# Kernel tuning notes

Measured on AMD Instinct MI355X. Metric: run time of the kernel, lower is better.

Reference implementation:

```python
import jax, jax.numpy as jnp
import numpy as np

N = 16384          # total points
B = 2              # scans; points[:,0] is batch id
K = 16             # knn neighbors (includes self, dist 0)
CH = [4, 16, 16, 32, 32]
EPS = 1e-5


def setup_inputs() -> dict:
    key = jax.random.key(0)
    ks = jax.random.split(key, 1 + len(CH) - 1)
    feat = jax.random.normal(ks[0], (N, 4), dtype=jnp.float32)
    bidx = jnp.repeat(jnp.arange(B, dtype=jnp.float32), N // B)
    points = jnp.concatenate([bidx[:, None], feat], axis=1)  # [N,5]
    inp = {"points": points}
    for i in range(len(CH) - 1):
        in_c, out_c = CH[i], CH[i + 1]
        inp[f"W{i}"] = jax.random.normal(ks[1 + i], (out_c, 2 * in_c), dtype=jnp.float32) * 0.1
        inp[f"b{i}"] = jnp.zeros((out_c,), dtype=jnp.float32)
        inp[f"g{i}"] = jnp.ones((out_c,), dtype=jnp.float32)
        inp[f"t{i}"] = jnp.zeros((out_c,), dtype=jnp.float32)
    return inp


def _knn(pos, bidx, k):
    # batched brute-force knn: mask cross-batch pairs with +inf
    d2 = jnp.sum(pos * pos, axis=-1)
    dist = d2[:, None] + d2[None, :] - 2.0 * (pos @ pos.T)  # [N,N]
    dist = jnp.where(bidx[:, None] == bidx[None, :], dist, jnp.inf)
    return jax.lax.top_k(-dist, k)[1]  # [N,k] indices of nearest


def _edge_conv(x, idx, W, b, g, t):
    # x: [N,C]; idx: [N,k]
    xi = x[:, None, :]                                   # [N,1,C]
    e = jnp.concatenate(
        [jnp.broadcast_to(xi, idx.shape + (x.shape[-1],)), x[idx] - xi], axis=-1
    )                                                    # [N,k,2C]
    h = jnp.einsum('nke,oe->nko', e, W) + b              # [N,k,out]
    mu = h.mean(axis=(0, 1))
    var = h.var(axis=(0, 1))
    h = (h - mu) * jax.lax.rsqrt(var + EPS) * g + t      # batch-norm (train mode)
    return jnp.max(jax.nn.relu(h), axis=1)               # max over neighbors -> [N,out]


def reference(points, W0, b0, g0, t0, W1, b1, g1, t1, W2, b2, g2, t2, W3, b3, g3, t3):
    bidx = points[:, 0].astype(jnp.int32)
    pos = points[:, 1:4]
    idx = _knn(pos, bidx, K)
    x = points[:, 1:]  # [N,4]
    for W, b, g, t in ((W0, b0, g0, t0), (W1, b1, g1, t1), (W2, b2, g2, t2), (W3, b3, g3, t3)):
        x = _edge_conv(x, idx, W, b, g, t)
    return x  # [N,32] == batch_dict['gcn_feature']
```

## Files before the change

kernel.cpp:

```cpp
#include <hip/hip_runtime.h>
#include <math.h>

typedef unsigned long long u64;

#define N_PTS 16384
#define HALF_N 8192
#define KK 16
#define NK (N_PTS * KK)
#define EPSV 1e-5f
#define FINF 0x7f800000u

#define TGRP 32
#define TGC 64
#define QW 2
#define QBLK 8
#define CAP 288

#define OFF_IDX   0u
#define OFF_PC    (1u << 20)
#define OFF_MA    (OFF_PC + N_PTS * 16u)
#define OFF_MB    (OFF_MA + N_PTS * 16u * 4u)
#define OFF_MC    (OFF_MB + N_PTS * 16u * 4u)
#define OFF_PART  (OFF_MC + N_PTS * 32u * 4u)
#define OFF_STATS (OFF_PART + 1024u * 64u * 4u)

__global__ __launch_bounds__(256) void prep_kernel(const float* __restrict__ pts,
                                                   float4* __restrict__ pc) {
    int i = blockIdx.x * 256 + threadIdx.x;
    float x = pts[i * 5 + 1], y = pts[i * 5 + 2], z = pts[i * 5 + 3];
    float d2 = __fadd_rn(__fadd_rn(__fmul_rn(x, x), __fmul_rn(y, y)), __fmul_rn(z, z));
    pc[i] = make_float4(x, y, z, d2);
}

__device__ __forceinline__ unsigned fkey(unsigned u) {
    return u ^ ((unsigned)(((int)u) >> 31) | 0x80000000u);
}

__device__ __forceinline__ void cef32(float& a, float& b) {
    float t = fminf(a, b);
    b = fmaxf(a, b);
    a = t;
}

__device__ __forceinline__ void sort8f(float* b) {
    cef32(b[0], b[1]); cef32(b[2], b[3]); cef32(b[4], b[5]); cef32(b[6], b[7]);
    cef32(b[0], b[2]); cef32(b[1], b[3]); cef32(b[4], b[6]); cef32(b[5], b[7]);
    cef32(b[1], b[2]); cef32(b[5], b[6]);
    cef32(b[0], b[4]); cef32(b[1], b[5]); cef32(b[2], b[6]); cef32(b[3], b[7]);
    cef32(b[2], b[4]); cef32(b[3], b[5]);
    cef32(b[1], b[2]); cef32(b[3], b[4]); cef32(b[5], b[6]);
}

__device__ __forceinline__ void sort16f(float b[16]) {
    sort8f(b); sort8f(b + 8);
#pragma unroll
    for (int j = 0; j < 8; ++j) cef32(b[j], b[15 - j]);
#pragma unroll
    for (int h = 0; h < 16; h += 8) {
        cef32(b[h + 0], b[h + 4]); cef32(b[h + 1], b[h + 5]);
        cef32(b[h + 2], b[h + 6]); cef32(b[h + 3], b[h + 7]);
        cef32(b[h + 0], b[h + 2]); cef32(b[h + 1], b[h + 3]);
        cef32(b[h + 4], b[h + 6]); cef32(b[h + 5], b[h + 7]);
        cef32(b[h + 0], b[h + 1]); cef32(b[h + 2], b[h + 3]);
        cef32(b[h + 4], b[h + 5]); cef32(b[h + 6], b[h + 7]);
    }
}

__global__ __launch_bounds__(256, 8) void tau1_kernel(const float4* __restrict__ pc,
                                                      float* __restrict__ gsubT) {
    const int qb = blockIdx.x >> 5;
    const int g  = blockIdx.x & (TGRP - 1);
    const int n  = qb * 256 + threadIdx.x;
    const int base = (n >= HALF_N) ? HALF_N : 0;
    const float4 p = pc[n];

    float m = __uint_as_float(FINF);
    const int c0 = base + g * TGC;
#pragma unroll 8
    for (int t = 0; t < TGC; ++t) {
        const float4 cp = pc[c0 + t];
        float dot = __fadd_rn(__fadd_rn(__fmul_rn(p.x, cp.x), __fmul_rn(p.y, cp.y)),
                              __fmul_rn(p.z, cp.z));
        float dist = __fsub_rn(__fadd_rn(p.w, cp.w), __fmul_rn(2.0f, dot));
        m = fminf(m, dist);
    }
    gsubT[g * N_PTS + n] = m;
}

__global__ __launch_bounds__(256, 4) void tau2_kernel(const float* __restrict__ gsubT,
                                                      float* __restrict__ tauArr) {
    const int n = blockIdx.x * 256 + threadIdx.x;
    float A[16], B[16];
#pragma unroll
    for (int g = 0; g < 16; ++g) A[g] = gsubT[g * N_PTS + n];
#pragma unroll
    for (int g = 0; g < 16; ++g) B[g] = gsubT[(16 + g) * N_PTS + n];
    sort16f(A);
    sort16f(B);
    float tau = __uint_as_float(0xff800000u);
#pragma unroll
    for (int j = 0; j < 16; ++j) tau = fmaxf(tau, fminf(A[j], B[15 - j]));
    tauArr[n] = tau;
}

__global__ __launch_bounds__(256, 8) void collect_kernel(const float4* __restrict__ pc,
                                                         const float* __restrict__ tauArr,
                                                         int* __restrict__ idx) {
    __shared__ u64 lists[QBLK][CAP];

    const int tid  = threadIdx.x;
    const int lane = tid & 63;
    const int w    = tid >> 6;
    const int nb   = blockIdx.x * QBLK + w * QW;
    const int base = (blockIdx.x >= (HALF_N / QBLK)) ? HALF_N : 0;

    const float4 q0 = pc[nb + 0], q1 = pc[nb + 1];
    const float tau0 = tauArr[nb + 0], tau1 = tauArr[nb + 1];

    u64* l0 = lists[w * QW + 0];
    u64* l1 = lists[w * QW + 1];
    int c0 = 0, c1 = 0;

    const u64 lt = (1ull << lane) - 1ull;

    for (int t0 = 0; t0 < HALF_N; t0 += 64) {
        const int ci = base + t0 + lane;
        const float4 cp = pc[ci];

#define DIST(Q) (__fsub_rn(__fadd_rn(Q.w, cp.w), __fmul_rn(2.0f,                      \
            __fadd_rn(__fadd_rn(__fmul_rn(Q.x, cp.x), __fmul_rn(Q.y, cp.y)),          \
                      __fmul_rn(Q.z, cp.z)))))
        const float d0 = DIST(q0);
        const float d1 = DIST(q1);
#undef DIST

#define APPEND(D, TAU, LST, CNT)                                                      \
        {                                                                             \
            const bool acc = !((D) > (TAU));                                          \
            const u64 mask = __ballot(acc);                                           \
            if (mask) {                                                               \
                if (acc) {                                                            \
                    int slot = (CNT) + (int)__popcll(mask & lt);                      \
                    if (slot < CAP)                                                   \
                        (LST)[slot] = ((u64)fkey(__float_as_uint(D)) << 32) | (unsigned)ci; \
                }                                                                     \
                (CNT) += (int)__popcll(mask);                                         \
            }                                                                         \
        }
        APPEND(d0, tau0, l0, c0)
        APPEND(d1, tau1, l1, c1)
#undef APPEND
    }

#define SELECT(LST, CNT, QI)                                                          \
    {                                                                                 \
        const int K = min((CNT), CAP);                                                \
        for (int e = lane; e < K; e += 64) {                                          \
            u64 my = (LST)[e];                                                        \
            int rank = 0;                                                             \
            for (int i = 0; i < K; ++i) rank += ((LST)[i] < my) ? 1 : 0;              \
            if (rank < 16) idx[(nb + (QI)) * KK + rank] = (int)(my & 0xffffffffULL);  \
        }                                                                             \
    }
    SELECT(l0, c0, 0)
    SELECT(l1, c1, 1)
#undef SELECT
}

template <int IN_C, int OUT_C, int MODE>
__global__ __launch_bounds__(256) void convS_kernel(const float* __restrict__ xin,
                                                    const float* __restrict__ statsPrev,
                                                    const int* __restrict__ idxg,
                                                    const float* __restrict__ W,
                                                    const float* __restrict__ bb,
                                                    float* __restrict__ part,
                                                    float* __restrict__ mout) {
    constexpr int RED = 256 / OUT_C;
    __shared__ float hbuf[OUT_C][257];
    __shared__ float pr1[OUT_C][RED + 1];
    __shared__ float pr2[OUT_C][RED + 1];
    __shared__ float2 sAB[IN_C];

    const int tid = threadIdx.x;
    const int gt = blockIdx.x * 256 + tid;
    const int n = gt >> 4;

    if (MODE == 1) {
        if (tid < IN_C) sAB[tid] = make_float2(statsPrev[tid], statsPrev[32 + tid]);
        __syncthreads();
    }

    float xn[IN_C], dx[IN_C];
    const int j = idxg[gt];
    if (MODE == 0) {
        const float* rn = xin + n * 5 + 1;
        const float* rj = xin + j * 5 + 1;
#pragma unroll
        for (int e = 0; e < IN_C; ++e) xn[e] = rn[e];
#pragma unroll
        for (int e = 0; e < IN_C; ++e) dx[e] = rj[e] - xn[e];
    } else {
        const float4* rn = (const float4*)(xin + n * IN_C);
        const float4* rj = (const float4*)(xin + j * IN_C);
#pragma unroll
        for (int e4 = 0; e4 < IN_C / 4; ++e4) {
            float4 a = rn[e4];
            float4 bq = rj[e4];
            float av[4] = {a.x, a.y, a.z, a.w};
            float bv[4] = {bq.x, bq.y, bq.z, bq.w};
#pragma unroll
            for (int u = 0; u < 4; ++u) {
                float2 ab = sAB[4 * e4 + u];
                float xv = fmaxf(fmaf(av[u], ab.x, ab.y), 0.f);
                float jv = fmaxf(fmaf(bv[u], ab.x, ab.y), 0.f);
                xn[4 * e4 + u] = xv;
                dx[4 * e4 + u] = jv - xv;
            }
        }
    }

    float h[OUT_C];
#pragma unroll
    for (int c = 0; c < OUT_C; ++c) {
        float acc = bb[c];
#pragma unroll
        for (int e = 0; e < IN_C; ++e) acc = fmaf(W[c * 2 * IN_C + e], xn[e], acc);
#pragma unroll
        for (int e = 0; e < IN_C; ++e) acc = fmaf(W[c * 2 * IN_C + IN_C + e], dx[e], acc);
        h[c] = acc;
    }

#pragma unroll
    for (int c = 0; c < OUT_C; ++c) hbuf[c][tid] = h[c];
    __syncthreads();
    {
        const int c2 = tid & (OUT_C - 1);
        const int ch = tid / OUT_C;
        float s1 = 0.f, s2 = 0.f;
#pragma unroll
        for (int i = 0; i < OUT_C; ++i) {
            float hh = hbuf[c2][ch * OUT_C + i];
            s1 += hh; s2 += hh * hh;
        }
        pr1[c2][ch] = s1;
        pr2[c2][ch] = s2;
    }
    __syncthreads();
    if (tid < OUT_C) {
        float t1 = 0.f, t2 = 0.f;
#pragma unroll
        for (int k = 0; k < RED; ++k) { t1 += pr1[tid][k]; t2 += pr2[tid][k]; }
        part[blockIdx.x * 64 + tid]      = t1;
        part[blockIdx.x * 64 + 32 + tid] = t2;
    }

    {
        const int n0 = blockIdx.x * 16;
        constexpr int ITER = OUT_C / 16;
#pragma unroll
        for (int r = 0; r < ITER; ++r) {
            const int c = tid & (OUT_C - 1);
            const int nl = (tid / OUT_C) + r * (256 / OUT_C);
            float m = hbuf[c][nl * 16];
#pragma unroll
            for (int k = 1; k < 16; ++k) m = fmaxf(m, hbuf[c][nl * 16 + k]);
            mout[(n0 + nl) * OUT_C + c] = m;
        }
    }
}

__global__ __launch_bounds__(256) void finalize_kernel(const float* __restrict__ part,
                                                       const float* __restrict__ g,
                                                       const float* __restrict__ t,
                                                       float* __restrict__ statsL) {
    __shared__ float s1[128], s2[128];
    const int c = blockIdx.x;
    const int tid = threadIdx.x;

    if (tid < 128) {
        float a = 0.f;
#pragma unroll
        for (int i = 0; i < 8; ++i) a += part[(tid * 8 + i) * 64 + c];
        s1[tid] = a;
    } else {
        const int t2 = tid - 128;
        float a = 0.f;
#pragma unroll
        for (int i = 0; i < 8; ++i) a += part[(t2 * 8 + i) * 64 + 32 + c];
        s2[t2] = a;
    }
    __syncthreads();
    for (int st = 64; st >= 1; st >>= 1) {
        if (tid < st) s1[tid] += s1[tid + st];
        else if (tid >= 128 && tid < 128 + st) s2[tid - 128] += s2[tid - 128 + st];
        __syncthreads();
    }
    if (tid == 0) {
        const float inv = 1.0f / (float)NK;
        float mu  = s1[0] * inv;
        float var = s2[0] * inv - mu * mu;
        float rs  = 1.0f / sqrtf(var + EPSV);
        float A   = rs * g[c];
        statsL[c]      = A;
        statsL[32 + c] = t[c] - mu * A;
    }
}

__global__ __launch_bounds__(256) void apply_kernel(const float* __restrict__ m,
                                                    const float* __restrict__ st,
                                                    float* __restrict__ out) {
    const int i = blockIdx.x * 256 + threadIdx.x;
    float4 mv = ((const float4*)m)[i];
    const int c0 = (i * 4) & 31;
    float4 Av = *(const float4*)(st + c0);
    float4 Bv = *(const float4*)(st + 32 + c0);
    float4 o;
    o.x = fmaxf(fmaf(mv.x, Av.x, Bv.x), 0.f);
    o.y = fmaxf(fmaf(mv.y, Av.y, Bv.y), 0.f);
    o.z = fmaxf(fmaf(mv.z, Av.z, Bv.z), 0.f);
    o.w = fmaxf(fmaf(mv.w, Av.w, Bv.w), 0.f);
    ((float4*)out)[i] = o;
}

extern "C" void kernel_launch(void* const* d_in, const int* in_sizes, int n_in,
                              void* d_out, int out_size, void* d_ws, size_t ws_size,
                              hipStream_t stream) {
    const float* pts = (const float*)d_in[0];
    const float* Wl[4], *bl[4], *gl[4], *tl[4];
    for (int l = 0; l < 4; ++l) {
        Wl[l] = (const float*)d_in[1 + 4 * l + 0];
        bl[l] = (const float*)d_in[1 + 4 * l + 1];
        gl[l] = (const float*)d_in[1 + 4 * l + 2];
        tl[l] = (const float*)d_in[1 + 4 * l + 3];
    }
    char* ws = (char*)d_ws;
    int*    idx    = (int*)(ws + OFF_IDX);
    float4* pc     = (float4*)(ws + OFF_PC);
    float*  gsubT  = (float*)(ws + OFF_MA);
    float*  m0     = (float*)(ws + OFF_MA);
    float*  m1     = (float*)(ws + OFF_MB);
    float*  m2     = (float*)(ws + OFF_MC);
    float*  m3     = (float*)(ws + OFF_MA);
    float*  part   = (float*)(ws + OFF_PART);
    float*  tauArr = (float*)(ws + OFF_PART);
    float*  stats  = (float*)(ws + OFF_STATS);
    float*  out    = (float*)d_out;

    prep_kernel<<<N_PTS / 256, 256, 0, stream>>>(pts, pc);
    tau1_kernel<<<(N_PTS / 256) * TGRP, 256, 0, stream>>>(pc, gsubT);
    tau2_kernel<<<N_PTS / 256, 256, 0, stream>>>(gsubT, tauArr);
    collect_kernel<<<N_PTS / QBLK, 256, 0, stream>>>(pc, tauArr, idx);

    const int GA = NK / 256;

    convS_kernel<4, 16, 0><<<GA, 256, 0, stream>>>(pts, nullptr, idx, Wl[0], bl[0], part, m0);
    finalize_kernel<<<16, 256, 0, stream>>>(part, gl[0], tl[0], stats + 0);

    convS_kernel<16, 16, 1><<<GA, 256, 0, stream>>>(m0, stats + 0, idx, Wl[1], bl[1], part, m1);
    finalize_kernel<<<16, 256, 0, stream>>>(part, gl[1], tl[1], stats + 64);

    convS_kernel<16, 32, 1><<<GA, 256, 0, stream>>>(m1, stats + 64, idx, Wl[2], bl[2], part, m2);
    finalize_kernel<<<32, 256, 0, stream>>>(part, gl[2], tl[2], stats + 128);

    convS_kernel<32, 32, 1><<<GA, 256, 0, stream>>>(m2, stats + 128, idx, Wl[3], bl[3], part, m3);
    finalize_kernel<<<32, 256, 0, stream>>>(part, gl[3], tl[3], stats + 192);

    apply_kernel<<<(N_PTS * 32 / 4) / 256, 256, 0, stream>>>(m3, stats + 192, out);
}
```

Baseline: 186.8 us.

## Fold tau selection into collect, prefetch candidates, share per-point weight term

The separate tau2 kernel is removed and each collect wave now computes its two query thresholds inline from the per-group minima, saving one launch and a round trip through global memory. The candidate loop software-prefetches the next point's coordinates so the load overlaps the distance and append work. In the edge-conv kernel, the W·x_i half of the product is computed once per point, split across the 16 neighbor threads and shared through LDS, instead of being recomputed by every neighbor thread. The costs are redundant tau sorting by all 64 lanes of each wave, extra register pressure in collect, and an added barrier and shared-memory array in convS.

```diff
diff --git a/kernel.cpp b/kernel.cpp
--- a/kernel.cpp
+++ b/kernel.cpp
@@ -64,6 +64,20 @@
         cef32(b[h + 0], b[h + 1]); cef32(b[h + 2], b[h + 3]);
         cef32(b[h + 4], b[h + 5]); cef32(b[h + 6], b[h + 7]);
     }
+}
+
+__device__ __forceinline__ float tau_of(const float* __restrict__ gsubT, int n) {
+    float A[16], B[16];
+#pragma unroll
+    for (int g = 0; g < 16; ++g) A[g] = gsubT[g * N_PTS + n];
+#pragma unroll
+    for (int g = 0; g < 16; ++g) B[g] = gsubT[(16 + g) * N_PTS + n];
+    sort16f(A);
+    sort16f(B);
+    float tau = __uint_as_float(0xff800000u);
+#pragma unroll
+    for (int j = 0; j < 16; ++j) tau = fmaxf(tau, fminf(A[j], B[15 - j]));
+    return tau;
 }
 
 __global__ __launch_bounds__(256, 8) void tau1_kernel(const float4* __restrict__ pc,
@@ -87,24 +101,8 @@
     gsubT[g * N_PTS + n] = m;
 }
 
-__global__ __launch_bounds__(256, 4) void tau2_kernel(const float* __restrict__ gsubT,
-                                                      float* __restrict__ tauArr) {
-    const int n = blockIdx.x * 256 + threadIdx.x;
-    float A[16], B[16];
-#pragma unroll
-    for (int g = 0; g < 16; ++g) A[g] = gsubT[g * N_PTS + n];
-#pragma unroll
-    for (int g = 0; g < 16; ++g) B[g] = gsubT[(16 + g) * N_PTS + n];
-    sort16f(A);
-    sort16f(B);
-    float tau = __uint_as_float(0xff800000u);
-#pragma unroll
-    for (int j = 0; j < 16; ++j) tau = fmaxf(tau, fminf(A[j], B[15 - j]));
-    tauArr[n] = tau;
-}
-
 __global__ __launch_bounds__(256, 8) void collect_kernel(const float4* __restrict__ pc,
-                                                         const float* __restrict__ tauArr,
+                                                         const float* __restrict__ gsubT,
                                                          int* __restrict__ idx) {
     __shared__ u64 lists[QBLK][CAP];
 
@@ -115,17 +113,21 @@
     const int base = (blockIdx.x >= (HALF_N / QBLK)) ? HALF_N : 0;
 
     const float4 q0 = pc[nb + 0], q1 = pc[nb + 1];
-    const float tau0 = tauArr[nb + 0], tau1 = tauArr[nb + 1];
+    const float tau0 = tau_of(gsubT, nb + 0);
+    const float tau1 = tau_of(gsubT, nb + 1);
 
     u64* l0 = lists[w * QW + 0];
     u64* l1 = lists[w * QW + 1];
     int c0 = 0, c1 = 0;
 
     const u64 lt = (1ull << lane) - 1ull;
-
+    const int ci_l = base + lane;
+
+    float4 cp = pc[ci_l];
     for (int t0 = 0; t0 < HALF_N; t0 += 64) {
-        const int ci = base + t0 + lane;
-        const float4 cp = pc[ci];
+        const int nt = (t0 + 64 < HALF_N) ? (t0 + 64) : t0;
+        const float4 nxt = pc[ci_l + nt];
+        const int ci = ci_l + t0;
 
 #define DIST(Q) (__fsub_rn(__fadd_rn(Q.w, cp.w), __fmul_rn(2.0f,                      \
             __fadd_rn(__fadd_rn(__fmul_rn(Q.x, cp.x), __fmul_rn(Q.y, cp.y)),          \
@@ -150,6 +152,7 @@
         APPEND(d0, tau0, l0, c0)
         APPEND(d1, tau1, l1, c1)
 #undef APPEND
+        cp = nxt;
     }
 
 #define SELECT(LST, CNT, QI)                                                          \
@@ -180,10 +183,13 @@
     __shared__ float pr1[OUT_C][RED + 1];
     __shared__ float pr2[OUT_C][RED + 1];
     __shared__ float2 sAB[IN_C];
+    __shared__ float accN[16][OUT_C + 1];
 
     const int tid = threadIdx.x;
     const int gt = blockIdx.x * 256 + tid;
     const int n = gt >> 4;
+    const int nl = tid >> 4;
+    const int kq = tid & 15;
 
     if (MODE == 1) {
         if (tid < IN_C) sAB[tid] = make_float2(statsPrev[tid], statsPrev[32 + tid]);
@@ -219,12 +225,23 @@
         }
     }
 
+    {
+        constexpr int CPO = OUT_C / 16;
+#pragma unroll
+        for (int u = 0; u < CPO; ++u) {
+            const int c = kq * CPO + u;
+            float acc = bb[c];
+#pragma unroll
+            for (int e = 0; e < IN_C; ++e) acc = fmaf(W[c * 2 * IN_C + e], xn[e], acc);
+            accN[nl][c] = acc;
+        }
+    }
+    __syncthreads();
+
     float h[OUT_C];
 #pragma unroll
     for (int c = 0; c < OUT_C; ++c) {
-        float acc = bb[c];
-#pragma unroll
-        for (int e = 0; e < IN_C; ++e) acc = fmaf(W[c * 2 * IN_C + e], xn[e], acc);
+        float acc = accN[nl][c];
 #pragma unroll
         for (int e = 0; e < IN_C; ++e) acc = fmaf(W[c * 2 * IN_C + IN_C + e], dx[e], acc);
         h[c] = acc;
@@ -260,11 +277,11 @@
 #pragma unroll
         for (int r = 0; r < ITER; ++r) {
             const int c = tid & (OUT_C - 1);
-            const int nl = (tid / OUT_C) + r * (256 / OUT_C);
-            float m = hbuf[c][nl * 16];
-#pragma unroll
-            for (int k = 1; k < 16; ++k) m = fmaxf(m, hbuf[c][nl * 16 + k]);
-            mout[(n0 + nl) * OUT_C + c] = m;
+            const int nl2 = (tid / OUT_C) + r * (256 / OUT_C);
+            float m = hbuf[c][nl2 * 16];
+#pragma unroll
+            for (int k = 1; k < 16; ++k) m = fmaxf(m, hbuf[c][nl2 * 16 + k]);
+            mout[(n0 + nl2) * OUT_C + c] = m;
         }
     }
 }
@@ -342,14 +359,12 @@
     float*  m2     = (float*)(ws + OFF_MC);
     float*  m3     = (float*)(ws + OFF_MA);
     float*  part   = (float*)(ws + OFF_PART);
-    float*  tauArr = (float*)(ws + OFF_PART);
     float*  stats  = (float*)(ws + OFF_STATS);
     float*  out    = (float*)d_out;
 
     prep_kernel<<<N_PTS / 256, 256, 0, stream>>>(pts, pc);
     tau1_kernel<<<(N_PTS / 256) * TGRP, 256, 0, stream>>>(pc, gsubT);
-    tau2_kernel<<<N_PTS / 256, 256, 0, stream>>>(gsubT, tauArr);
-    collect_kernel<<<N_PTS / QBLK, 256, 0, stream>>>(pc, tauArr, idx);
+    collect_kernel<<<N_PTS / QBLK, 256, 0, stream>>>(pc, gsubT, idx);
 
     const int GA = NK / 256;
 
```

New measurement: 214.8 us. 15.0% more time.
